# Optimization experiments

Hardware: AMD Instinct MI355X
Metric: run time of the kernel (lower is better)

## Reference

```python
import jax, jax.numpy as jnp
import numpy as np

N = 1_000_000   # detections
FDIM = 64       # embedding dim
C = 128         # number of clusters (track ids in [0, C))
DELTA_VAR = 0.5
DELTA_DIST = 3.0


def setup_inputs() -> dict:
    key = jax.random.key(0)
    k1, k2 = jax.random.split(key)
    features = jax.random.normal(k1, (N, FDIM), dtype=jnp.float32)
    labels = jax.random.randint(k2, (N, 2), 0, C, dtype=jnp.int32)  # [fr, track_id], all ids >= 0
    return {"features": features, "labels": labels}


def reference(features, labels):
    # All track ids are >= 0 by construction, so the tp_ids filter is a no-op
    # and the dynamic unique-cluster loop becomes a fixed-C segment reduce.
    ids = labels[:, 1]
    ones = jnp.ones((features.shape[0],), dtype=features.dtype)
    counts = jax.ops.segment_sum(ones, ids, num_segments=C)            # (C,)
    sums = jax.ops.segment_sum(features, ids, num_segments=C)         # (C, F)
    means = sums / counts[:, None]                                     # per-cluster mean

    # variance term: per-point distance to its cluster mean, hinged at delta_var
    d = jnp.linalg.norm(features - means[ids], axis=1)                 # (N,)
    per_pt = jnp.square(jax.nn.relu(d - DELTA_VAR))
    per_cluster = jax.ops.segment_sum(per_pt, ids, num_segments=C) / counts
    var_loss = jnp.sum(per_cluster) / C

    # pairwise cluster-distance term over i != j, hinged at delta_dist
    diff = means[:, None, :] - means[None, :, :]                       # (C, C, F)
    sq = jnp.sum(diff * diff, axis=-1)                                 # (C, C)
    eye = jnp.eye(C, dtype=bool)
    pd = jnp.sqrt(jnp.where(eye, 1.0, sq))                             # safe sqrt on diagonal
    dl = jnp.where(eye, 0.0, jnp.square(jax.nn.relu(DELTA_DIST - pd)))
    dist_loss = jnp.sum(dl) / (C * (C - 1))

    return var_loss + dist_loss
```

## Files before the change

### kernel.cpp

```cpp
#include <hip/hip_runtime.h>

#define NPTS 1000000
#define FDIM 64
#define CNUM 128
#define PSTRIDE 8320
#define NB1 1280
#define NB3 1024

typedef _Float16 half8 __attribute__((ext_vector_type(8)));
typedef float f32x4 __attribute__((ext_vector_type(4)));

__global__ __launch_bounds__(256, 5) void k1_partials(
    const float* __restrict__ feats, const int* __restrict__ labels,
    float* __restrict__ partials, int nblocks)
{
    __shared__ float cnt[CNUM];
    const int tid = threadIdx.x;
    if (tid < CNUM) cnt[tid] = 0.f;
    __syncthreads();

    const int lane = tid & 63;
    const int n15 = lane & 15;
    const int kb = (lane >> 4) * 8;
    const int rowb = (lane >> 4) * 4;
    const int fq = tid >> 6;
    const int fbase = fq * 16;

    f32x4 acc[8];
    #pragma unroll
    for (int ct = 0; ct < 8; ++ct) acc[ct] = (f32x4){0.f, 0.f, 0.f, 0.f};

    const int ntiles = NPTS / 32;
    int t = blockIdx.x;
    float fv[8]; int vl[8]; int cl = 0;
    if (t < ntiles) {
        const int p0 = t * 32;
        const float* fp = feats + (size_t)(p0 + kb) * FDIM + fbase + n15;
        const int* lp = labels + 2 * (p0 + kb) + 1;
        #pragma unroll
        for (int i = 0; i < 8; ++i) fv[i] = fp[i * FDIM];
        #pragma unroll
        for (int i = 0; i < 8; ++i) vl[i] = lp[2 * i];
        if (lane < 32) cl = labels[2 * (p0 + lane) + 1];
    }
    while (t < ntiles) {
        const int tn = t + nblocks;
        float fv2[8]; int vl2[8]; int cl2 = 0;
        if (tn < ntiles) {
            const int p0 = tn * 32;
            const float* fp = feats + (size_t)(p0 + kb) * FDIM + fbase + n15;
            const int* lp = labels + 2 * (p0 + kb) + 1;
            #pragma unroll
            for (int i = 0; i < 8; ++i) fv2[i] = fp[i * FDIM];
            #pragma unroll
            for (int i = 0; i < 8; ++i) vl2[i] = lp[2 * i];
            if (lane < 32) cl2 = labels[2 * (p0 + lane) + 1];
        }
        if (fq == 0 && lane < 32) atomicAdd(&cnt[cl], 1.0f);

        half8 B;
        #pragma unroll
        for (int i = 0; i < 8; ++i) B[i] = (_Float16)fv[i];
        #pragma unroll
        for (int ct = 0; ct < 8; ++ct) {
            const int cmine = ct * 16 + n15;
            union { unsigned u[4]; half8 h; } ua;
            #pragma unroll
            for (int j = 0; j < 4; ++j)
                ua.u[j] = ((vl[2 * j] == cmine) ? 0x3C00u : 0u)
                        | ((vl[2 * j + 1] == cmine) ? 0x3C000000u : 0u);
            acc[ct] = __builtin_amdgcn_mfma_f32_16x16x32_f16(ua.h, B, acc[ct], 0, 0, 0);
        }
        t = tn;
        #pragma unroll
        for (int i = 0; i < 8; ++i) { fv[i] = fv2[i]; vl[i] = vl2[i]; }
        cl = cl2;
    }
    __syncthreads();

    float* dst = partials + (size_t)blockIdx.x * PSTRIDE;
    #pragma unroll
    for (int ct = 0; ct < 8; ++ct)
        #pragma unroll
        for (int reg = 0; reg < 4; ++reg) {
            const int c = ct * 16 + rowb + reg;
            dst[c * FDIM + fbase + n15] = acc[ct][reg];
        }
    if (tid < CNUM) dst[8192 + tid] = cnt[tid];
}

__global__ __launch_bounds__(256) void k2_reduce(
    const float* __restrict__ partials, int nblocks, float* __restrict__ red,
    float* __restrict__ ppsum, float* __restrict__ dsum, int* __restrict__ counter)
{
    const int tid = threadIdx.x;
    const int tsub = tid & 15, grp = tid >> 4;
    const int t0 = blockIdx.x * 16;
    float s = 0.f;
    #pragma unroll 8
    for (int b = grp; b < nblocks; b += 16)
        s += partials[(size_t)b * PSTRIDE + t0 + tsub];
    __shared__ float lred[16][17];
    lred[grp][tsub] = s;
    __syncthreads();
    if (tid < 16) {
        float tot = 0.f;
        #pragma unroll
        for (int q = 0; q < 16; ++q) tot += lred[q][tid];
        red[t0 + tid] = tot;
    }
    if (blockIdx.x == 0) {
        if (tid >= 128) ppsum[tid - 128] = 0.f;
        if (tid == 64) dsum[0] = 0.f;
        if (tid == 65) counter[0] = 0;
    }
}

__global__ __launch_bounds__(256, 4) void k3_var(
    const float4* __restrict__ feats4, const int* __restrict__ labels,
    const float* __restrict__ red, float* __restrict__ ppsum, int nblocks)
{
    __shared__ float4 mu4[CNUM * 16];
    __shared__ float lpp[CNUM];
    const int tid = threadIdx.x;
    for (int i = tid; i < 2048; i += 256) {
        float4 sv = ((const float4*)red)[i];
        float ci = 1.0f / red[8192 + (i >> 4)];
        mu4[i] = make_float4(sv.x * ci, sv.y * ci, sv.z * ci, sv.w * ci);
    }
    if (tid < CNUM) lpp[tid] = 0.f;
    __syncthreads();

    const int lane = tid & 63;
    const int k = lane & 15, g = lane >> 4;
    const int nwaves = nblocks * 4;
    const int wid = ((blockIdx.x << 8) + tid) >> 6;
    const int ntiles = NPTS / 16;

    int b = wid;
    float4 v[4]; int cc = 0;
    if (b < ntiles) {
        const float4* fp = feats4 + (size_t)b * 256 + lane;
        #pragma unroll
        for (int s = 0; s < 4; ++s) v[s] = fp[s * 64];
        cc = labels[2 * (b * 16 + k) + 1];
    }
    while (b < ntiles) {
        const int bn = b + nwaves;
        float4 vn[4]; int ccn = 0;
        if (bn < ntiles) {
            const float4* fp = feats4 + (size_t)bn * 256 + lane;
            #pragma unroll
            for (int s = 0; s < 4; ++s) vn[s] = fp[s * 64];
            ccn = labels[2 * (bn * 16 + k) + 1];
        }
        #pragma unroll
        for (int s = 0; s < 4; ++s) {
            const int c = __shfl(cc, 4 * s + g);
            float4 m = mu4[c * 16 + k];
            float dx = v[s].x - m.x, dy = v[s].y - m.y,
                  dz = v[s].z - m.z, dw = v[s].w - m.w;
            float sq = dx * dx + dy * dy + dz * dz + dw * dw;
            sq += __shfl_xor(sq, 1); sq += __shfl_xor(sq, 2);
            sq += __shfl_xor(sq, 4); sq += __shfl_xor(sq, 8);
            if (k == 0) {
                const float t = sqrtf(sq) - 0.5f;
                if (t > 0.f) atomicAdd(&lpp[c], t * t);
            }
        }
        b = bn;
        #pragma unroll
        for (int s = 0; s < 4; ++s) v[s] = vn[s];
        cc = ccn;
    }
    __syncthreads();
    if (tid < CNUM) atomicAdd(&ppsum[tid], lpp[tid]);
}

__global__ __launch_bounds__(128) void k45_dist_final(
    const float* __restrict__ red, const float* __restrict__ ppsum,
    float* __restrict__ dsum, int* __restrict__ counter, float* __restrict__ out)
{
    __shared__ float4 mu4[CNUM * 17];
    __shared__ int lastflag;
    __shared__ float sv[2];
    const int tid = threadIdx.x;
    for (int i = tid; i < 2048; i += 128) {
        float4 s4 = ((const float4*)red)[i];
        float ci = 1.0f / red[8192 + (i >> 4)];
        mu4[(i >> 4) * 17 + (i & 15)] =
            make_float4(s4.x * ci, s4.y * ci, s4.z * ci, s4.w * ci);
    }
    __syncthreads();
    const int i = blockIdx.x, j = tid;
    float sq = 0.f;
    #pragma unroll
    for (int q = 0; q < 16; ++q) {
        float4 a = mu4[i * 17 + q], b = mu4[j * 17 + q];
        float dx = a.x - b.x, dy = a.y - b.y, dz = a.z - b.z, dw = a.w - b.w;
        sq += dx * dx + dy * dy + dz * dz + dw * dw;
    }
    float dl = 0.f;
    if (j != i) {
        const float r = 3.0f - sqrtf(sq);
        if (r > 0.f) dl = r * r;
    }
    #pragma unroll
    for (int m = 1; m < 64; m <<= 1) dl += __shfl_xor(dl, m);
    if ((tid & 63) == 0) atomicAdd(dsum, dl);
    __threadfence();
    __syncthreads();
    if (tid == 0) lastflag = (atomicAdd(counter, 1) == (int)gridDim.x - 1);
    __syncthreads();
    if (lastflag) {
        float v = ppsum[tid] / red[8192 + tid];
        #pragma unroll
        for (int m = 1; m < 64; m <<= 1) v += __shfl_xor(v, m);
        if ((tid & 63) == 0) sv[tid >> 6] = v;
    }
    __syncthreads();
    if (lastflag && tid == 0) {
        const float dtot = atomicAdd(dsum, 0.0f);
        out[0] = (sv[0] + sv[1]) / (float)CNUM
               + dtot / (float)(CNUM * (CNUM - 1));
    }
}

extern "C" void kernel_launch(void* const* d_in, const int* in_sizes, int n_in,
                              void* d_out, int out_size, void* d_ws, size_t ws_size,
                              hipStream_t stream) {
    (void)in_sizes; (void)n_in; (void)out_size;
    const float* feats   = (const float*)d_in[0];
    const float4* feats4 = (const float4*)d_in[0];
    const int* labels    = (const int*)d_in[1];
    float* ws            = (float*)d_ws;
    float* out           = (float*)d_out;

    int nb1 = NB1;
    {
        size_t avail = ws_size / sizeof(float);
        size_t fixed = PSTRIDE + 128 + 2;
        if (avail > fixed) {
            size_t cap = (avail - fixed) / PSTRIDE;
            if ((size_t)nb1 > cap) nb1 = (int)cap;
        } else nb1 = 1;
        if (nb1 < 1) nb1 = 1;
    }
    float* partials = ws;
    float* red      = ws + (size_t)nb1 * PSTRIDE;
    float* ppsum    = red + PSTRIDE;
    float* dsum     = ppsum + 128;
    int*   counter  = (int*)(dsum + 1);

    k1_partials<<<nb1, 256, 0, stream>>>(feats, labels, partials, nb1);
    k2_reduce<<<PSTRIDE / 16, 256, 0, stream>>>(partials, nb1, red, ppsum, dsum, counter);
    k3_var<<<NB3, 256, 0, stream>>>(feats4, labels, red, ppsum, NB3);
    k45_dist_final<<<CNUM, 128, 0, stream>>>(red, ppsum, dsum, counter, out);
}
```

Before: 149.6 us.

## Split cluster rows across waves instead of feature columns in partial-sum kernel

The work split inside each k1 block is re-partitioned. Before, each wave owned a 16-wide feature slice and all 128 clusters. Now each wave owns 32 clusters (two 16-row one-hot tiles) and all 64 features, so each wave builds only two one-hot masks per tile instead of eight. The cost is that every wave now loads the full 32x64 feature tile, so the block issues four times the feature loads and relies on L1/L2 to absorb the duplicates. Register use also grows, so the grid size and the launch-bounds occupancy hint are lowered to match.

```diff
diff --git a/kernel.cpp b/kernel.cpp
--- a/kernel.cpp
+++ b/kernel.cpp
@@ -4,13 +4,13 @@
 #define FDIM 64
 #define CNUM 128
 #define PSTRIDE 8320
-#define NB1 1280
+#define NB1 1024
 #define NB3 1024
 
 typedef _Float16 half8 __attribute__((ext_vector_type(8)));
 typedef float f32x4 __attribute__((ext_vector_type(4)));
 
-__global__ __launch_bounds__(256, 5) void k1_partials(
+__global__ __launch_bounds__(256, 4) void k1_partials(
     const float* __restrict__ feats, const int* __restrict__ labels,
     float* __restrict__ partials, int nblocks)
 {
@@ -23,69 +23,85 @@
     const int n15 = lane & 15;
     const int kb = (lane >> 4) * 8;
     const int rowb = (lane >> 4) * 4;
-    const int fq = tid >> 6;
-    const int fbase = fq * 16;
-
-    f32x4 acc[8];
-    #pragma unroll
-    for (int ct = 0; ct < 8; ++ct) acc[ct] = (f32x4){0.f, 0.f, 0.f, 0.f};
+    const int w = tid >> 6;
+
+    f32x4 acc[2][4];
+    #pragma unroll
+    for (int ci = 0; ci < 2; ++ci)
+        #pragma unroll
+        for (int nt = 0; nt < 4; ++nt)
+            acc[ci][nt] = (f32x4){0.f, 0.f, 0.f, 0.f};
 
     const int ntiles = NPTS / 32;
     int t = blockIdx.x;
-    float fv[8]; int vl[8]; int cl = 0;
+
+    half8 B[4]; int vl[8]; int cl = 0;
     if (t < ntiles) {
         const int p0 = t * 32;
-        const float* fp = feats + (size_t)(p0 + kb) * FDIM + fbase + n15;
+        const float* fp = feats + (size_t)(p0 + kb) * FDIM + n15;
         const int* lp = labels + 2 * (p0 + kb) + 1;
         #pragma unroll
-        for (int i = 0; i < 8; ++i) fv[i] = fp[i * FDIM];
+        for (int nt = 0; nt < 4; ++nt)
+            #pragma unroll
+            for (int i = 0; i < 8; ++i)
+                B[nt][i] = (_Float16)fp[i * FDIM + nt * 16];
         #pragma unroll
         for (int i = 0; i < 8; ++i) vl[i] = lp[2 * i];
-        if (lane < 32) cl = labels[2 * (p0 + lane) + 1];
+        if (w == 0 && lane < 32) cl = labels[2 * (p0 + lane) + 1];
     }
     while (t < ntiles) {
         const int tn = t + nblocks;
-        float fv2[8]; int vl2[8]; int cl2 = 0;
+        float fv2[32]; int vl2[8]; int cl2 = 0;
         if (tn < ntiles) {
             const int p0 = tn * 32;
-            const float* fp = feats + (size_t)(p0 + kb) * FDIM + fbase + n15;
+            const float* fp = feats + (size_t)(p0 + kb) * FDIM + n15;
             const int* lp = labels + 2 * (p0 + kb) + 1;
             #pragma unroll
-            for (int i = 0; i < 8; ++i) fv2[i] = fp[i * FDIM];
+            for (int nt = 0; nt < 4; ++nt)
+                #pragma unroll
+                for (int i = 0; i < 8; ++i)
+                    fv2[nt * 8 + i] = fp[i * FDIM + nt * 16];
             #pragma unroll
             for (int i = 0; i < 8; ++i) vl2[i] = lp[2 * i];
-            if (lane < 32) cl2 = labels[2 * (p0 + lane) + 1];
-        }
-        if (fq == 0 && lane < 32) atomicAdd(&cnt[cl], 1.0f);
-
-        half8 B;
-        #pragma unroll
-        for (int i = 0; i < 8; ++i) B[i] = (_Float16)fv[i];
-        #pragma unroll
-        for (int ct = 0; ct < 8; ++ct) {
-            const int cmine = ct * 16 + n15;
+            if (w == 0 && lane < 32) cl2 = labels[2 * (p0 + lane) + 1];
+        }
+        if (w == 0 && lane < 32) atomicAdd(&cnt[cl], 1.0f);
+
+        #pragma unroll
+        for (int ci = 0; ci < 2; ++ci) {
+            const int cmine = (2 * w + ci) * 16 + n15;
             union { unsigned u[4]; half8 h; } ua;
             #pragma unroll
             for (int j = 0; j < 4; ++j)
                 ua.u[j] = ((vl[2 * j] == cmine) ? 0x3C00u : 0u)
                         | ((vl[2 * j + 1] == cmine) ? 0x3C000000u : 0u);
-            acc[ct] = __builtin_amdgcn_mfma_f32_16x16x32_f16(ua.h, B, acc[ct], 0, 0, 0);
+            #pragma unroll
+            for (int nt = 0; nt < 4; ++nt)
+                acc[ci][nt] = __builtin_amdgcn_mfma_f32_16x16x32_f16(
+                    ua.h, B[nt], acc[ci][nt], 0, 0, 0);
         }
         t = tn;
         #pragma unroll
-        for (int i = 0; i < 8; ++i) { fv[i] = fv2[i]; vl[i] = vl2[i]; }
+        for (int nt = 0; nt < 4; ++nt)
+            #pragma unroll
+            for (int i = 0; i < 8; ++i)
+                B[nt][i] = (_Float16)fv2[nt * 8 + i];
+        #pragma unroll
+        for (int i = 0; i < 8; ++i) vl[i] = vl2[i];
         cl = cl2;
     }
     __syncthreads();
 
     float* dst = partials + (size_t)blockIdx.x * PSTRIDE;
     #pragma unroll
-    for (int ct = 0; ct < 8; ++ct)
-        #pragma unroll
-        for (int reg = 0; reg < 4; ++reg) {
-            const int c = ct * 16 + rowb + reg;
-            dst[c * FDIM + fbase + n15] = acc[ct][reg];
-        }
+    for (int ci = 0; ci < 2; ++ci)
+        #pragma unroll
+        for (int nt = 0; nt < 4; ++nt)
+            #pragma unroll
+            for (int reg = 0; reg < 4; ++reg) {
+                const int c = (2 * w + ci) * 16 + rowb + reg;
+                dst[c * FDIM + nt * 16 + n15] = acc[ci][nt][reg];
+            }
     if (tid < CNUM) dst[8192 + tid] = cnt[tid];
 }
 
```

Result: slower. 156.4 us (+4.5%).
